# Kernel optimization log

Hardware: AMD Instinct MI355X
Metric: run time of the kernel (lower is better)

The kernel has to match this reference:

```python
import jax, jax.numpy as jnp
import numpy as np

EPS = 1e-12  # matches torch F.normalize eps


def _l2norm(t):
    n = jnp.linalg.norm(t, axis=-1, keepdims=True)
    return t / jnp.maximum(n, EPS)


def setup_inputs() -> dict:
    key = jax.random.key(0)
    ks = jax.random.split(key, 10)
    B, N, C = 2, 2048, 384
    nH, hd = 12, 32
    inp = {
        "x": jax.random.normal(ks[0], (B, N, C), jnp.float32),
        "q_w": jax.random.normal(ks[1], (C, C), jnp.float32) * 0.02,
        "q_b": jax.random.normal(ks[2], (C,), jnp.float32) * 0.02,
        "kv_w": jax.random.normal(ks[3], (2 * C, C), jnp.float32) * 0.02,
        "kv_b": jax.random.normal(ks[4], (2 * C,), jnp.float32) * 0.02,
        "query_embedding": jax.random.normal(ks[5], (nH, 1, hd), jnp.float32) * 0.02,
        # init of temperature in torch: log(exp(1/0.24) - 1)
        "temperature": jnp.full((nH, 1, 1), float(np.log(np.exp(1.0 / 0.24) - 1.0)), jnp.float32),
        "pos_bias": jax.random.normal(ks[7], (nH, N), jnp.float32) * 0.0004,
        "proj_w": jax.random.normal(ks[8], (C, C), jnp.float32) * 0.02,
        "proj_b": jax.random.normal(ks[9], (C,), jnp.float32) * 0.02,
        "D": 8, "H": 16, "W": 16,
    }
    return inp


def reference(x, q_w, q_b, kv_w, kv_b, query_embedding, temperature, pos_bias, proj_w, proj_b, D, H, W):
    B, N, C = x.shape
    nH, hd = query_embedding.shape[0], query_embedding.shape[2]
    assert N == D * H * W
    # q projection -> [B, nH, N, hd], cosine-normalized
    q = (x @ q_w.T + q_b).reshape(B, N, nH, hd).transpose(0, 2, 1, 3)
    q = _l2norm(q)
    # additive query embedding, softplus temperature, seq-length (log N) scale
    scale = jax.nn.softplus(temperature) * jnp.float32(np.log(N))  # [nH,1,1]
    q = (q + query_embedding[None]) * scale[None]
    # kv projection
    kv = x @ kv_w.T + kv_b  # [B, N, 2C]
    k, v = kv[..., :C], kv[..., C:]
    k = _l2norm(k.reshape(B, N, nH, hd).transpose(0, 2, 1, 3))
    v = v.reshape(B, N, nH, hd).transpose(0, 2, 1, 3)
    # scores with per-head learned positional bias over keys
    attn = jnp.einsum("bhqd,bhkd->bhqk", q, k) + pos_bias[None, :, None, :]
    attn = jax.nn.softmax(attn, axis=-1)
    out = jnp.einsum("bhqk,bhkd->bhqd", attn, v)
    out = out.transpose(0, 2, 1, 3).reshape(B, N, C)
    return out @ proj_w.T + proj_b
```

## Files before the change

kernel.cpp:

```cpp
#include <hip/hip_runtime.h>

#define LOG2E 1.4426950408889634f

typedef __bf16 bf16x8 __attribute__((ext_vector_type(8)));
typedef short s16x4 __attribute__((ext_vector_type(4)));
typedef float f32x4 __attribute__((ext_vector_type(4)));

#define BB 2
#define NN 2048
#define CC 384
#define NH 12
#define HD 32
#define MROWS (BB * NN)

__device__ __forceinline__ unsigned short f2bf(float f) {
  __bf16 h = (__bf16)f;
  return __builtin_bit_cast(unsigned short, h);
}

__device__ __forceinline__ bf16x8 ldg_bf8(const unsigned short* p) {
  uint4 v = *reinterpret_cast<const uint4*>(p);
  return __builtin_bit_cast(bf16x8, v);
}

__device__ __forceinline__ float fexp2(float x) {
#if __has_builtin(__builtin_amdgcn_exp2f)
  return __builtin_amdgcn_exp2f(x);
#else
  return exp2f(x);
#endif
}

__device__ __forceinline__ s16x4 pack_bf4(float a, float b, float c, float d) {
#if __has_builtin(__builtin_amdgcn_cvt_pk_bf16_f32)
  auto lo = __builtin_amdgcn_cvt_pk_bf16_f32(a, b);
  auto hi = __builtin_amdgcn_cvt_pk_bf16_f32(c, d);
  uint2 u = {__builtin_bit_cast(unsigned int, lo),
             __builtin_bit_cast(unsigned int, hi)};
  return __builtin_bit_cast(s16x4, u);
#else
  s16x4 r = {(short)f2bf(a), (short)f2bf(b), (short)f2bf(c), (short)f2bf(d)};
  return r;
#endif
}

typedef __attribute__((address_space(1))) const void gas_void;
typedef __attribute__((address_space(3))) void las_void;
__device__ __forceinline__ void gload_lds16(const void* g, void* l) {
  __builtin_amdgcn_global_load_lds((gas_void*)(unsigned long long)g,
                                   (las_void*)(unsigned long long)l, 16, 0, 0);
}

__device__ __forceinline__ f32x4 mfma32(bf16x8 a, bf16x8 b, f32x4 c) {
  return __builtin_amdgcn_mfma_f32_16x16x32_bf16(a, b, c, 0, 0, 0);
}

__device__ __forceinline__ f32x4 mfma16(s16x4 a, s16x4 b, f32x4 c) {
#if defined(__HIP_DEVICE_COMPILE__)
#if __has_builtin(__builtin_amdgcn_mfma_f32_16x16x16bf16_1k)
  return __builtin_amdgcn_mfma_f32_16x16x16bf16_1k(a, b, c, 0, 0, 0);
#else
  asm volatile("v_mfma_f32_16x16x16_bf16 %0, %1, %2, %0"
               : "+v"(c) : "v"(a), "v"(b));
  return c;
#endif
#else
  return c;
#endif
}

__global__ __launch_bounds__(256) void prep_kernel(
    const float* __restrict__ x, const float* __restrict__ q_w,
    const float* __restrict__ kv_w, const float* __restrict__ proj_w,
    const float* __restrict__ pos_bias, unsigned short* __restrict__ xb,
    unsigned short* __restrict__ qwb, unsigned short* __restrict__ kvwb,
    unsigned short* __restrict__ pwb, float* __restrict__ bias2) {
  long i = (long)(blockIdx.x * 256 + threadIdx.x) * 8;
  auto cast8 = [&](const float* s, unsigned short* d, long off) {
    float4 a = *reinterpret_cast<const float4*>(s + off);
    float4 b = *reinterpret_cast<const float4*>(s + off + 4);
    s16x4 lo = pack_bf4(a.x, a.y, a.z, a.w);
    s16x4 hi = pack_bf4(b.x, b.y, b.z, b.w);
    uint2 l = __builtin_bit_cast(uint2, lo), h = __builtin_bit_cast(uint2, hi);
    uint4 o = {l.x, l.y, h.x, h.y};
    *reinterpret_cast<uint4*>(d + off) = o;
  };
  if (i < 1572864) { cast8(x, xb, i); return; }
  i -= 1572864;
  if (i < 147456) { cast8(q_w, qwb, i); return; }
  i -= 147456;
  if (i < 294912) { cast8(kv_w, kvwb, i); return; }
  i -= 294912;
  if (i < 147456) { cast8(proj_w, pwb, i); return; }
  i -= 147456;
  float4 a = *reinterpret_cast<const float4*>(pos_bias + i);
  float4 b = *reinterpret_cast<const float4*>(pos_bias + i + 4);
  a.x *= LOG2E; a.y *= LOG2E; a.z *= LOG2E; a.w *= LOG2E;
  b.x *= LOG2E; b.y *= LOG2E; b.z *= LOG2E; b.w *= LOG2E;
  *reinterpret_cast<float4*>(bias2 + i) = a;
  *reinterpret_cast<float4*>(bias2 + i + 4) = b;
}

__global__ __launch_bounds__(256, 4) void gemm_qkv_norm_kernel(
    const unsigned short* __restrict__ xb, const unsigned short* __restrict__ qwb,
    const unsigned short* __restrict__ kvwb, const float* __restrict__ q_b,
    const float* __restrict__ kv_b, const float* __restrict__ qe,
    const float* __restrict__ temperature, unsigned short* __restrict__ Qs,
    unsigned short* __restrict__ Kn, unsigned short* __restrict__ VT) {
  __shared__ alignas(16) char smem[2][20480];
  int wave = threadIdx.x >> 6, lane = threadIdx.x & 63;
  int c = lane & 15, quad = lane >> 4;
  int h = blockIdx.y;
  int m0b = blockIdx.x * 64;
  int cid = wave * 64 + lane;

  auto stage = [&](int buf, int kk) {
    char* base = smem[buf];
#pragma unroll
    for (int j = 0; j < 2; ++j) {
      int chunk = j * 256 + cid;
      int row = chunk >> 3, e = chunk & 7;
      gload_lds16(xb + (long)(m0b + row) * CC + kk + (e ^ (row & 7)) * 8,
                  base + j * 4096 + wave * 1024);
    }
#pragma unroll
    for (int j = 0; j < 3; ++j) {
      int chunk = j * 256 + cid;
      int row = chunk >> 3, e = chunk & 7;
      const unsigned short* src;
      if (row < 32)      src = qwb + (long)(h * 32 + row) * CC;
      else if (row < 64) src = kvwb + (long)(h * 32 + (row - 32)) * CC;
      else               src = kvwb + (long)(CC + h * 32 + (row - 64)) * CC;
      gload_lds16(src + kk + (e ^ (row & 7)) * 8,
                  base + 8192 + j * 4096 + wave * 1024);
    }
  };

  f32x4 acc[6] = {};
  auto compute = [&](int buf) {
    const char* base = smem[buf];
#pragma unroll
    for (int kh = 0; kh < 2; ++kh) {
      int sa = ((kh * 4 + quad) ^ (c & 7)) * 16;
      bf16x8 a = *(const bf16x8*)(base + (wave * 16 + c) * 128 + sa);
#pragma unroll
      for (int t = 0; t < 6; ++t) {
        bf16x8 b = *(const bf16x8*)(base + 8192 + (t * 16 + c) * 128 + sa);
        acc[t] = mfma32(a, b, acc[t]);
      }
    }
  };

  stage(0, 0);
#pragma unroll 1
  for (int s = 0; s < 6; ++s) {
    __syncthreads();
    if (s < 5) stage((s + 1) & 1, (s + 1) * 64);
    compute(s & 1);
  }

  int m0 = m0b + wave * 16;
  float qb0 = q_b[h * 32 + c], qb1 = q_b[h * 32 + 16 + c];
  float kb0 = kv_b[h * 32 + c], kb1 = kv_b[h * 32 + 16 + c];
  float vb0 = kv_b[CC + h * 32 + c], vb1 = kv_b[CC + h * 32 + 16 + c];
  float qe0 = qe[h * HD + c], qe1 = qe[h * HD + 16 + c];
  float sc = log1pf(expf(temperature[h])) * 11.0f;
  int b = m0 >> 11;
  int nb = (m0 & 2047) + quad * 4;
  int pair = b * NH + h;
  unsigned short* qsb = Qs + ((long)pair * NN + nb) * HD;
  unsigned short* knb = Kn + ((long)pair * NN + nb) * HD;
  ushort4 vp0, vp1;
#pragma unroll
  for (int r = 0; r < 4; ++r) {
    float q0 = acc[0][r] + qb0, q1 = acc[1][r] + qb1;
    float k0 = acc[2][r] + kb0, k1 = acc[3][r] + kb1;
    float v0 = acc[4][r] + vb0, v1 = acc[5][r] + vb1;
    float qs = q0 * q0 + q1 * q1, ks = k0 * k0 + k1 * k1;
#pragma unroll
    for (int off = 8; off; off >>= 1) {
      qs += __shfl_xor(qs, off);
      ks += __shfl_xor(ks, off);
    }
    float qi = 1.0f / fmaxf(sqrtf(qs), 1e-12f);
    float ki = 1.0f / fmaxf(sqrtf(ks), 1e-12f);
    qsb[r * HD + c] = f2bf((q0 * qi + qe0) * sc);
    qsb[r * HD + 16 + c] = f2bf((q1 * qi + qe1) * sc);
    knb[r * HD + c] = f2bf(k0 * ki);
    knb[r * HD + 16 + c] = f2bf(k1 * ki);
    ((unsigned short*)&vp0)[r] = f2bf(v0);
    ((unsigned short*)&vp1)[r] = f2bf(v1);
  }
  *reinterpret_cast<ushort4*>(VT + ((long)pair * HD + c) * NN + nb) = vp0;
  *reinterpret_cast<ushort4*>(VT + ((long)pair * HD + 16 + c) * NN + nb) = vp1;
}

__global__ __launch_bounds__(256, 4) void attn_kernel(
    const unsigned short* __restrict__ Qs, const unsigned short* __restrict__ Kn,
    const unsigned short* __restrict__ VT, const float* __restrict__ bias2,
    unsigned short* __restrict__ ao) {
  __shared__ alignas(16) char smem[2][16384];
  __shared__ alignas(16) char biasl[8192];
  int wave = threadIdx.x >> 6, lane = threadIdx.x & 63;
  int c = lane & 15, quad = lane >> 4;
  int id = blockIdx.x;
  int xcd = id & 7, rr = id >> 3;
  int pair = (rr >> 5) * 8 + xcd;
  int qt = rr & 31;
  int h = pair % NH, b = pair / NH;
  const unsigned short* Qp = Qs + (long)pair * NN * HD;
  const char* Kg0 = (const char*)(Kn + (long)pair * NN * HD);
  const char* Vg0 = (const char*)(VT + (long)pair * HD * NN);
  const char* bp = (const char*)(bias2 + h * NN);
  int q0 = qt * 64 + wave * 16;
  bf16x8 qf = ldg_bf8(Qp + (long)(q0 + c) * HD + quad * 8);
  f32x4 o0 = {}, o1 = {};
  float rs = 0.f;

  const int koff = (c * 4 + quad) * 16;

  auto stage = [&](int buf, int i) {
    char* tb = smem[buf];
    long krow0 = (long)i * 128;
    const char* Kg = Kg0 + krow0 * (HD * 2);
    const char* Vg = Vg0 + krow0 * 2;
#pragma unroll
    for (int j = 0; j < 2; ++j) {
      int ck = wave * 2 + j;
      gload_lds16(Kg + ck * 1024 + koff, tb + ck * 1024);
      int chunk = ck * 64 + lane;
      int d = chunk >> 4, e = chunk & 15;
      int es = e ^ (d & 15);
      gload_lds16(Vg + (long)d * (NN * 2) + es * 16, tb + 8192 + ck * 1024);
    }
  };

  auto compute = [&](int buf, int i) {
    const char* kb = smem[buf] + lane * 16;
    const char* vb = smem[buf] + 8192;
    const char* bl = biasl + i * 512 + quad * 16;
#pragma unroll
    for (int t8 = 0; t8 < 8; ++t8) {
      bf16x8 kf = *(const bf16x8*)(kb + t8 * 1024);
      f32x4 bbv = *(const f32x4*)(bl + t8 * 64);
      f32x4 s = mfma32(kf, qf, bbv);
      float p0 = fexp2(s[0]);
      float p1 = fexp2(s[1]);
      float p2 = fexp2(s[2]);
      float p3 = fexp2(s[3]);
      rs += (p0 + p1) + (p2 + p3);
      s16x4 pf = pack_bf4(p0, p1, p2, p3);
      int vsw = (((t8 * 2 + (quad >> 1)) ^ c) * 16) + (quad & 1) * 8;
      s16x4 vlo = *(const s16x4*)(vb + c * 256 + vsw);
      s16x4 vhi = *(const s16x4*)(vb + (c + 16) * 256 + vsw);
      o0 = mfma16(vlo, pf, o0);
      o1 = mfma16(vhi, pf, o1);
    }
  };

#pragma unroll
  for (int j = 0; j < 2; ++j)
    gload_lds16(bp + j * 4096 + wave * 1024 + lane * 16,
                biasl + j * 4096 + wave * 1024);
  stage(0, 0);

#pragma unroll 1
  for (int i = 0; i < 16; ++i) {
    asm volatile("s_waitcnt lgkmcnt(0)" ::: "memory");
    __builtin_amdgcn_s_barrier();
    if (i < 15) {
      stage((i + 1) & 1, i + 1);
      asm volatile("s_waitcnt vmcnt(4)" ::: "memory");
    } else {
      asm volatile("s_waitcnt vmcnt(0)" ::: "memory");
    }
    __builtin_amdgcn_s_barrier();
    __builtin_amdgcn_sched_barrier(0);
    __builtin_amdgcn_s_setprio(1);
    compute(i & 1, i);
    __builtin_amdgcn_s_setprio(0);
  }

  rs += __shfl_xor(rs, 16);
  rs += __shfl_xor(rs, 32);
  float inv = 1.0f / rs;
  unsigned short* op = ao + (long)(b * NN + q0 + c) * CC + h * HD + quad * 4;
  ushort4 s0, s1;
#pragma unroll
  for (int r = 0; r < 4; ++r) {
    ((unsigned short*)&s0)[r] = f2bf(o0[r] * inv);
    ((unsigned short*)&s1)[r] = f2bf(o1[r] * inv);
  }
  *reinterpret_cast<ushort4*>(op) = s0;
  *reinterpret_cast<ushort4*>(op + 16) = s1;
}

__global__ __launch_bounds__(256, 4) void proj_kernel(
    const unsigned short* __restrict__ ab, const unsigned short* __restrict__ pwb,
    const float* __restrict__ proj_b, float* __restrict__ out) {
  __shared__ alignas(16) char smem[2][12288];
  int wave = threadIdx.x >> 6, lane = threadIdx.x & 63;
  int c = lane & 15, quad = lane >> 4;
  int m0b = blockIdx.x * 64;
  int n0 = blockIdx.y * 32;
  int cid = wave * 64 + lane;

  auto stage = [&](int buf, int kk) {
    char* base = smem[buf];
#pragma unroll
    for (int j = 0; j < 2; ++j) {
      int chunk = j * 256 + cid;
      int row = chunk >> 3, e = chunk & 7;
      gload_lds16(ab + (long)(m0b + row) * CC + kk + (e ^ (row & 7)) * 8,
                  base + j * 4096 + wave * 1024);
    }
    {
      int row = cid >> 3, e = cid & 7;
      gload_lds16(pwb + (long)(n0 + row) * CC + kk + (e ^ (row & 7)) * 8,
                  base + 8192 + wave * 1024);
    }
  };

  f32x4 acc[2] = {};
  auto compute = [&](int buf) {
    const char* base = smem[buf];
#pragma unroll
    for (int kh = 0; kh < 2; ++kh) {
      int sa = ((kh * 4 + quad) ^ (c & 7)) * 16;
      bf16x8 a = *(const bf16x8*)(base + (wave * 16 + c) * 128 + sa);
#pragma unroll
      for (int t = 0; t < 2; ++t) {
        bf16x8 b = *(const bf16x8*)(base + 8192 + (t * 16 + c) * 128 + sa);
        acc[t] = mfma32(a, b, acc[t]);
      }
    }
  };

  stage(0, 0);
#pragma unroll 1
  for (int s = 0; s < 6; ++s) {
    __syncthreads();
    if (s < 5) stage((s + 1) & 1, (s + 1) * 64);
    compute(s & 1);
  }

  int m0 = m0b + wave * 16;
#pragma unroll
  for (int t = 0; t < 2; ++t) {
    int o = n0 + t * 16 + c;
    float bv = proj_b[o];
#pragma unroll
    for (int r = 0; r < 4; ++r) {
      out[(long)(m0 + quad * 4 + r) * CC + o] = acc[t][r] + bv;
    }
  }
}

extern "C" void kernel_launch(void* const* d_in, const int* in_sizes, int n_in,
                              void* d_out, int out_size, void* d_ws, size_t ws_size,
                              hipStream_t stream) {
  const float* x = (const float*)d_in[0];
  const float* q_w = (const float*)d_in[1];
  const float* q_b = (const float*)d_in[2];
  const float* kv_w = (const float*)d_in[3];
  const float* kv_b = (const float*)d_in[4];
  const float* qe = (const float*)d_in[5];
  const float* temp = (const float*)d_in[6];
  const float* pos_bias = (const float*)d_in[7];
  const float* proj_w = (const float*)d_in[8];
  const float* proj_b = (const float*)d_in[9];
  float* out = (float*)d_out;

  char* ws = (char*)d_ws;
  unsigned short* xb = (unsigned short*)(ws + 0);
  unsigned short* qwb = (unsigned short*)(ws + 3145728);
  unsigned short* kvwb = (unsigned short*)(ws + 3440640);
  unsigned short* pwb = (unsigned short*)(ws + 4030464);
  unsigned short* Qs = (unsigned short*)(ws + 4325376);
  unsigned short* Kn = (unsigned short*)(ws + 7471104);
  unsigned short* VT = (unsigned short*)(ws + 10616832);
  unsigned short* ao = (unsigned short*)(ws + 13762560);
  float* bias2 = (float*)(ws + 16908288);

  prep_kernel<<<1068, 256, 0, stream>>>(x, q_w, kv_w, proj_w, pos_bias, xb, qwb,
                                        kvwb, pwb, bias2);
  gemm_qkv_norm_kernel<<<dim3(64, NH), 256, 0, stream>>>(xb, qwb, kvwb, q_b, kv_b,
                                                         qe, temp, Qs, Kn, VT);
  attn_kernel<<<768, 256, 0, stream>>>(Qs, Kn, VT, bias2, ao);
  proj_kernel<<<dim3(64, 12), 256, 0, stream>>>(ao, pwb, proj_b, out);
}
```

Measured before the change: 127.2 us.

## Split attention keys across waves instead of queries, combine partials in LDS

Each wave now owns all 64 query rows of the block but only a quarter of the key range (a split-K over keys). It streams its own private K/V tiles, so the per-iteration block barriers are gone, and it reduces partial outputs and row sums across waves through LDS at the end. This removes the barrier synchronisation in the main loop and lets each K/V fragment be reused across four query fragments. In exchange it needs more registers (launch bounds drop to 3 blocks per CU) and adds an epilogue reduction through shared memory.

Result: faster. 124.7 us (-2.0%).

```diff
diff --git a/kernel.cpp b/kernel.cpp
--- a/kernel.cpp
+++ b/kernel.cpp
@@ -195,12 +195,11 @@
   *reinterpret_cast<ushort4*>(VT + ((long)pair * HD + 16 + c) * NN + nb) = vp1;
 }
 
-__global__ __launch_bounds__(256, 4) void attn_kernel(
+__global__ __launch_bounds__(256, 3) void attn_kernel(
     const unsigned short* __restrict__ Qs, const unsigned short* __restrict__ Kn,
     const unsigned short* __restrict__ VT, const float* __restrict__ bias2,
     unsigned short* __restrict__ ao) {
-  __shared__ alignas(16) char smem[2][16384];
-  __shared__ alignas(16) char biasl[8192];
+  __shared__ alignas(16) char smem[40960];
   int wave = threadIdx.x >> 6, lane = threadIdx.x & 63;
   int c = lane & 15, quad = lane >> 4;
   int id = blockIdx.x;
@@ -209,87 +208,120 @@
   int qt = rr & 31;
   int h = pair % NH, b = pair / NH;
   const unsigned short* Qp = Qs + (long)pair * NN * HD;
-  const char* Kg0 = (const char*)(Kn + (long)pair * NN * HD);
-  const char* Vg0 = (const char*)(VT + (long)pair * HD * NN);
+  const char* Kg0 = (const char*)(Kn + (long)pair * NN * HD) + wave * 32768;
+  const char* Vg0 = (const char*)(VT + (long)pair * HD * NN) + wave * 1024;
   const char* bp = (const char*)(bias2 + h * NN);
-  int q0 = qt * 64 + wave * 16;
-  bf16x8 qf = ldg_bf8(Qp + (long)(q0 + c) * HD + quad * 8);
-  f32x4 o0 = {}, o1 = {};
-  float rs = 0.f;
-
+  int q0 = qt * 64;
+  bf16x8 qf0 = ldg_bf8(Qp + (long)(q0 + c) * HD + quad * 8);
+  bf16x8 qf1 = ldg_bf8(Qp + (long)(q0 + 16 + c) * HD + quad * 8);
+  bf16x8 qf2 = ldg_bf8(Qp + (long)(q0 + 32 + c) * HD + quad * 8);
+  bf16x8 qf3 = ldg_bf8(Qp + (long)(q0 + 48 + c) * HD + quad * 8);
+  f32x4 o00 = {}, o10 = {}, o01 = {}, o11 = {};
+  f32x4 o02 = {}, o12 = {}, o03 = {}, o13 = {};
+  float rs0 = 0.f, rs1 = 0.f, rs2 = 0.f, rs3 = 0.f;
+
+  char* sw = smem + wave * 8192;
+  char* biasl = smem + 32768;
   const int koff = (c * 4 + quad) * 16;
+  int vd = lane >> 2, ve = lane & 3;
+  int ves = ve ^ (vd & 3);
 
   auto stage = [&](int buf, int i) {
-    char* tb = smem[buf];
-    long krow0 = (long)i * 128;
-    const char* Kg = Kg0 + krow0 * (HD * 2);
-    const char* Vg = Vg0 + krow0 * 2;
+    char* tb = sw + buf * 4096;
+    const char* Kg = Kg0 + i * 2048;
+    const char* Vg = Vg0 + i * 64;
 #pragma unroll
     for (int j = 0; j < 2; ++j) {
-      int ck = wave * 2 + j;
-      gload_lds16(Kg + ck * 1024 + koff, tb + ck * 1024);
-      int chunk = ck * 64 + lane;
-      int d = chunk >> 4, e = chunk & 15;
-      int es = e ^ (d & 15);
-      gload_lds16(Vg + (long)d * (NN * 2) + es * 16, tb + 8192 + ck * 1024);
-    }
-  };
+      gload_lds16(Kg + j * 1024 + koff, tb + j * 1024);
+      gload_lds16(Vg + (long)(j * 16 + vd) * (NN * 2) + ves * 16,
+                  tb + 2048 + j * 1024);
+    }
+  };
+
+#define FRAG_STEP(QF, O0, O1, RS)              \
+  {                                            \
+    f32x4 s = mfma32(kf, QF, bbv);             \
+    float p0 = fexp2(s[0]), p1 = fexp2(s[1]);  \
+    float p2 = fexp2(s[2]), p3 = fexp2(s[3]);  \
+    RS += (p0 + p1) + (p2 + p3);               \
+    s16x4 pf = pack_bf4(p0, p1, p2, p3);       \
+    O0 = mfma16(vlo, pf, O0);                  \
+    O1 = mfma16(vhi, pf, O1);                  \
+  }
 
   auto compute = [&](int buf, int i) {
-    const char* kb = smem[buf] + lane * 16;
-    const char* vb = smem[buf] + 8192;
-    const char* bl = biasl + i * 512 + quad * 16;
-#pragma unroll
-    for (int t8 = 0; t8 < 8; ++t8) {
+    const char* kb = sw + buf * 4096 + lane * 16;
+    const char* vb = sw + buf * 4096 + 2048;
+    const char* bl = biasl + wave * 2048 + i * 128 + quad * 16;
+#pragma unroll
+    for (int t8 = 0; t8 < 2; ++t8) {
       bf16x8 kf = *(const bf16x8*)(kb + t8 * 1024);
       f32x4 bbv = *(const f32x4*)(bl + t8 * 64);
-      f32x4 s = mfma32(kf, qf, bbv);
-      float p0 = fexp2(s[0]);
-      float p1 = fexp2(s[1]);
-      float p2 = fexp2(s[2]);
-      float p3 = fexp2(s[3]);
-      rs += (p0 + p1) + (p2 + p3);
-      s16x4 pf = pack_bf4(p0, p1, p2, p3);
-      int vsw = (((t8 * 2 + (quad >> 1)) ^ c) * 16) + (quad & 1) * 8;
-      s16x4 vlo = *(const s16x4*)(vb + c * 256 + vsw);
-      s16x4 vhi = *(const s16x4*)(vb + (c + 16) * 256 + vsw);
-      o0 = mfma16(vlo, pf, o0);
-      o1 = mfma16(vhi, pf, o1);
-    }
-  };
+      int sl = ((t8 * 2 + (quad >> 1)) ^ (c & 3)) * 16 + (quad & 1) * 8;
+      s16x4 vlo = *(const s16x4*)(vb + c * 64 + sl);
+      s16x4 vhi = *(const s16x4*)(vb + 1024 + c * 64 + sl);
+      FRAG_STEP(qf0, o00, o10, rs0)
+      FRAG_STEP(qf1, o01, o11, rs1)
+      FRAG_STEP(qf2, o02, o12, rs2)
+      FRAG_STEP(qf3, o03, o13, rs3)
+    }
+  };
+#undef FRAG_STEP
 
 #pragma unroll
   for (int j = 0; j < 2; ++j)
     gload_lds16(bp + j * 4096 + wave * 1024 + lane * 16,
                 biasl + j * 4096 + wave * 1024);
   stage(0, 0);
+  __syncthreads();
 
 #pragma unroll 1
   for (int i = 0; i < 16; ++i) {
     asm volatile("s_waitcnt lgkmcnt(0)" ::: "memory");
-    __builtin_amdgcn_s_barrier();
     if (i < 15) {
       stage((i + 1) & 1, i + 1);
       asm volatile("s_waitcnt vmcnt(4)" ::: "memory");
     } else {
       asm volatile("s_waitcnt vmcnt(0)" ::: "memory");
     }
-    __builtin_amdgcn_s_barrier();
     __builtin_amdgcn_sched_barrier(0);
-    __builtin_amdgcn_s_setprio(1);
     compute(i & 1, i);
-    __builtin_amdgcn_s_setprio(0);
-  }
-
-  rs += __shfl_xor(rs, 16);
-  rs += __shfl_xor(rs, 32);
-  float inv = 1.0f / rs;
-  unsigned short* op = ao + (long)(b * NN + q0 + c) * CC + h * HD + quad * 4;
+  }
+
+  __syncthreads();
+  float* comb = (float*)smem;
+#define PUT(F, O0, O1, RS)                                          \
+  {                                                                 \
+    float* p = comb + ((F * 4 + wave) * 9) * 64 + lane;             \
+    p[0] = O0[0]; p[64] = O0[1]; p[128] = O0[2]; p[192] = O0[3];    \
+    p[256] = O1[0]; p[320] = O1[1]; p[384] = O1[2]; p[448] = O1[3]; \
+    p[512] = RS;                                                    \
+  }
+  PUT(0, o00, o10, rs0)
+  PUT(1, o01, o11, rs1)
+  PUT(2, o02, o12, rs2)
+  PUT(3, o03, o13, rs3)
+#undef PUT
+  __syncthreads();
+  f32x4 A0 = {}, A1 = {};
+  float AR = 0.f;
+#pragma unroll
+  for (int w2 = 0; w2 < 4; ++w2) {
+    const float* p = comb + ((wave * 4 + w2) * 9) * 64 + lane;
+    A0[0] += p[0]; A0[1] += p[64]; A0[2] += p[128]; A0[3] += p[192];
+    A1[0] += p[256]; A1[1] += p[320]; A1[2] += p[384]; A1[3] += p[448];
+    AR += p[512];
+  }
+  AR += __shfl_xor(AR, 16);
+  AR += __shfl_xor(AR, 32);
+  float inv = 1.0f / AR;
+  int qr = q0 + wave * 16 + c;
+  unsigned short* op = ao + (long)(b * NN + qr) * CC + h * HD + quad * 4;
   ushort4 s0, s1;
 #pragma unroll
   for (int r = 0; r < 4; ++r) {
-    ((unsigned short*)&s0)[r] = f2bf(o0[r] * inv);
-    ((unsigned short*)&s1)[r] = f2bf(o1[r] * inv);
+    ((unsigned short*)&s0)[r] = f2bf(A0[r] * inv);
+    ((unsigned short*)&s1)[r] = f2bf(A1[r] * inv);
   }
   *reinterpret_cast<ushort4*>(op) = s0;
   *reinterpret_cast<ushort4*>(op + 16) = s1;
```
